# Optimization experiments

Hardware: AMD Instinct MI355X
Metric: run time of the kernel (lower is better)

## Reference

```python
import jax, jax.numpy as jnp
import numpy as np

N_NODES = 40000
N_EDGES = 640000
IN_DIM = 128
HID = 128
NCLS = 10
N_GRAPHS = 16
K = 2  # DGL TAGConv default number of hops


def setup_inputs() -> dict:
    key = jax.random.key(0)
    ks = jax.random.split(key, 8)
    h = jax.random.normal(ks[0], (N_NODES, IN_DIM), dtype=jnp.float32)
    src = jax.random.randint(ks[1], (N_EDGES,), 0, N_NODES, dtype=jnp.int64)
    dst = jax.random.randint(ks[2], (N_EDGES,), 0, N_NODES, dtype=jnp.int64)
    graph_ids = jnp.sort(jax.random.randint(ks[3], (N_NODES,), 0, N_GRAPHS, dtype=jnp.int64))
    # Xavier-ish scaled params
    W1 = jax.random.normal(ks[4], ((K + 1) * IN_DIM, HID), dtype=jnp.float32) / np.sqrt((K + 1) * IN_DIM)
    b1 = jnp.zeros((HID,), dtype=jnp.float32)
    W2 = jax.random.normal(ks[5], ((K + 1) * HID, HID), dtype=jnp.float32) / np.sqrt((K + 1) * HID)
    b2 = jnp.zeros((HID,), dtype=jnp.float32)
    Wc = jax.random.normal(ks[6], (HID, NCLS), dtype=jnp.float32) / np.sqrt(HID)
    bc = jnp.zeros((NCLS,), dtype=jnp.float32)
    return {"h": h, "src": src, "dst": dst, "graph_ids": graph_ids,
            "W1": W1, "b1": b1, "W2": W2, "b2": b2, "Wc": Wc, "bc": bc}


def _tagconv(x, src, dst, norm, W, b):
    feats = [x]
    for _ in range(K):
        msg = (x * norm)[src]                                   # [E, d] gather D^{-1/2} x at src
        x = norm * jax.ops.segment_sum(msg, dst, num_segments=norm.shape[0])  # scatter-sum to dst
        feats.append(x)
    return jax.nn.relu(jnp.concatenate(feats, axis=-1) @ W + b)


def reference(h, src, dst, graph_ids, W1, b1, W2, b2, Wc, bc):
    n = h.shape[0]
    deg = jax.ops.segment_sum(jnp.ones(src.shape[0], h.dtype), dst, num_segments=n)
    norm = jnp.maximum(deg, 1.0) ** -0.5  # D^{-1/2} with clamp(min=1), as in DGL
    norm = norm[:, None]
    x = _tagconv(h, src, dst, norm, W1, b1)
    x = _tagconv(x, src, dst, norm, W2, b2)
    pooled = jax.ops.segment_max(x, graph_ids, num_segments=N_GRAPHS)  # [G, HID] per-graph max pool
    return pooled @ Wc + bc  # [G, NCLS]
```

## Files before the change

### kernel.cpp

```cpp
#include <hip/hip_runtime.h>
#include <hip/hip_bf16.h>

#define NN 40000
#define NE 640000
#define HID 128
#define NCLS 10
#define NGRAPH 16

typedef __attribute__((ext_vector_type(8))) short bf16x8;
typedef __attribute__((ext_vector_type(4))) float f32x4;

__device__ inline float bf2f(unsigned short u) {
    unsigned int x = ((unsigned int)u) << 16;
    return __builtin_bit_cast(float, x);
}
__device__ inline unsigned short f2bf(float f) {
    __hip_bfloat16 h = __float2bfloat16(f);
    return __builtin_bit_cast(unsigned short, h);
}

__global__ void k_count_deg(const int* __restrict__ dst, int* __restrict__ deg, int n) {
    int e = blockIdx.x * blockDim.x + threadIdx.x;
    if (e < n) atomicAdd(&deg[__builtin_nontemporal_load(dst + e)], 1);
}

__global__ __launch_bounds__(1024) void k_scan1(const int* __restrict__ deg, int* __restrict__ row_start,
                                                int* __restrict__ partial, float* __restrict__ norm) {
    __shared__ int wsum[16];
    int tid = threadIdx.x, lane = tid & 63, wid = tid >> 6;
    int i = blockIdx.x * 1024 + tid;
    int v = (i < NN) ? deg[i] : 0;
    if (i < NN) norm[i] = rsqrtf(fmaxf((float)v, 1.0f));
    int sv = v;
    #pragma unroll
    for (int off = 1; off < 64; off <<= 1) {
        int t = __shfl_up(sv, off);
        if (lane >= off) sv += t;
    }
    if (lane == 63) wsum[wid] = sv;
    __syncthreads();
    if (wid == 0) {
        int ws = (lane < 16) ? wsum[lane] : 0;
        #pragma unroll
        for (int off = 1; off < 16; off <<= 1) {
            int t = __shfl_up(ws, off);
            if (lane >= off) ws += t;
        }
        if (lane < 16) wsum[lane] = ws;
    }
    __syncthreads();
    int excl = (wid > 0 ? wsum[wid - 1] : 0) + (sv - v);
    if (i < NN) row_start[i] = excl;
    if (tid == 0) partial[blockIdx.x] = wsum[15];
}

__global__ __launch_bounds__(1024) void k_scan3(int* __restrict__ row_start, const int* __restrict__ partial,
                                                int* __restrict__ cursor, int nb) {
    __shared__ int sh_carry, sh_all;
    int tid = threadIdx.x;
    if (tid < 64) {
        int v = (tid < nb) ? partial[tid] : 0;
        int lt = (tid < (int)blockIdx.x) ? v : 0;
        #pragma unroll
        for (int off = 32; off; off >>= 1) {
            lt += __shfl_down(lt, off);
            v  += __shfl_down(v, off);
        }
        if (tid == 0) { sh_carry = lt; sh_all = v; }
    }
    __syncthreads();
    int i = blockIdx.x * 1024 + tid;
    if (i < NN) {
        int val = row_start[i] + sh_carry;
        row_start[i] = val;
        cursor[i] = val;
    }
    if (blockIdx.x == 0 && tid == 0) row_start[NN] = sh_all;
}

__global__ void k_fill_csr(const int* __restrict__ src, const int* __restrict__ dst,
                           int* __restrict__ cursor, int* __restrict__ csr_src, int n) {
    int e = blockIdx.x * blockDim.x + threadIdx.x;
    if (e < n) {
        int d = __builtin_nontemporal_load(dst + e);
        int sv = __builtin_nontemporal_load(src + e);
        int pos = atomicAdd(&cursor[d], 1);
        csr_src[pos] = sv;
    }
}

__global__ void k_cvt_h(const float* __restrict__ h, unsigned short* __restrict__ hb) {
    int i = blockIdx.x * 256 + threadIdx.x;
    if (i < NN * HID / 4) {
        float4 v = reinterpret_cast<const float4*>(h)[i];
        ushort4 o;
        o.x = f2bf(v.x); o.y = f2bf(v.y); o.z = f2bf(v.z); o.w = f2bf(v.w);
        reinterpret_cast<ushort4*>(hb)[i] = o;
    }
}

__global__ void k_cvt_wt(const float* __restrict__ W1, const float* __restrict__ W2,
                         unsigned short* __restrict__ W1t, unsigned short* __restrict__ W2t) {
    int t = blockIdx.x * 256 + threadIdx.x;
    const float* W = blockIdx.y ? W2 : W1;
    unsigned short* Wt = blockIdx.y ? W2t : W1t;
    if (t < 384 * HID) {
        int c = t / 384, k = t % 384;
        Wt[t] = f2bf(W[(size_t)k * HID + c]);
    }
}

__global__ __launch_bounds__(256) void k_prop_bf(const unsigned short* __restrict__ x, const float* __restrict__ norm,
                                                 const int* __restrict__ row_start, const int* __restrict__ csr_src,
                                                 unsigned short* __restrict__ y) {
    int node = blockIdx.x * 4 + threadIdx.y;
    int lane = threadIdx.x;
    int h = lane >> 5;
    int sub = lane & 31;
    int colb = sub * 4;
    float a0 = 0.f, a1 = 0.f, a2 = 0.f, a3 = 0.f;
    int s = row_start[node], e = row_start[node + 1];
    int i = s + h;
    if (i + 6 < e) {
        int c0 = csr_src[i], c1 = csr_src[i + 2], c2 = csr_src[i + 4], c3 = csr_src[i + 6];
        int j = i + 8;
        while (true) {
            bool more = (j + 6 < e);
            int n0, n1, n2, n3;
            if (more) {
                n0 = csr_src[j]; n1 = csr_src[j + 2]; n2 = csr_src[j + 4]; n3 = csr_src[j + 6];
            }
            float s0 = norm[c0], s1 = norm[c1], s2 = norm[c2], s3 = norm[c3];
            ushort4 v0 = *reinterpret_cast<const ushort4*>(x + (size_t)c0 * HID + colb);
            ushort4 v1 = *reinterpret_cast<const ushort4*>(x + (size_t)c1 * HID + colb);
            ushort4 v2 = *reinterpret_cast<const ushort4*>(x + (size_t)c2 * HID + colb);
            ushort4 v3 = *reinterpret_cast<const ushort4*>(x + (size_t)c3 * HID + colb);
            a0 += s0 * bf2f(v0.x) + s1 * bf2f(v1.x) + s2 * bf2f(v2.x) + s3 * bf2f(v3.x);
            a1 += s0 * bf2f(v0.y) + s1 * bf2f(v1.y) + s2 * bf2f(v2.y) + s3 * bf2f(v3.y);
            a2 += s0 * bf2f(v0.z) + s1 * bf2f(v1.z) + s2 * bf2f(v2.z) + s3 * bf2f(v3.z);
            a3 += s0 * bf2f(v0.w) + s1 * bf2f(v1.w) + s2 * bf2f(v2.w) + s3 * bf2f(v3.w);
            i = j;
            if (!more) break;
            c0 = n0; c1 = n1; c2 = n2; c3 = n3;
            j += 8;
        }
    }
    for (; i < e; i += 2) {
        int sn = csr_src[i];
        float ns = norm[sn];
        ushort4 v = *reinterpret_cast<const ushort4*>(x + (size_t)sn * HID + colb);
        a0 += ns * bf2f(v.x); a1 += ns * bf2f(v.y); a2 += ns * bf2f(v.z); a3 += ns * bf2f(v.w);
    }
    a0 += __shfl_xor(a0, 32);
    a1 += __shfl_xor(a1, 32);
    a2 += __shfl_xor(a2, 32);
    a3 += __shfl_xor(a3, 32);
    if (h == 0) {
        float nd = norm[node];
        ushort4 o;
        o.x = f2bf(nd * a0); o.y = f2bf(nd * a1); o.z = f2bf(nd * a2); o.w = f2bf(nd * a3);
        *reinterpret_cast<ushort4*>(y + (size_t)node * HID + colb) = o;
    }
}

__global__ __launch_bounds__(128) void k_gemm_mfma(const unsigned short* __restrict__ x0,
                                                   const unsigned short* __restrict__ x1,
                                                   const unsigned short* __restrict__ x2,
                                                   const unsigned short* __restrict__ Wt,
                                                   const float* __restrict__ bias,
                                                   unsigned short* __restrict__ y) {
    int tid = threadIdx.x;
    int wave = tid >> 6;
    int lane = tid & 63;
    int r = lane & 15, kg = lane >> 4;
    int row0 = blockIdx.x * 32 + wave * 16;
    const unsigned short* xs[3] = { x0, x1, x2 };

    f32x4 acc[8];
    #pragma unroll
    for (int cf = 0; cf < 8; ++cf) acc[cf] = (f32x4){0.f, 0.f, 0.f, 0.f};

    #pragma unroll
    for (int kseg = 0; kseg < 3; ++kseg) {
        const unsigned short* __restrict__ xp = xs[kseg] + (size_t)(row0 + r) * HID;
        #pragma unroll
        for (int kb = 0; kb < 4; ++kb) {
            bf16x8 afrag = *reinterpret_cast<const bf16x8*>(xp + kb * 32 + kg * 8);
            #pragma unroll
            for (int cf = 0; cf < 8; ++cf) {
                bf16x8 bfrag = *reinterpret_cast<const bf16x8*>(
                    Wt + (size_t)(cf * 16 + r) * 384 + kseg * 128 + kb * 32 + kg * 8);
                acc[cf] = __builtin_amdgcn_mfma_f32_16x16x32_bf16(afrag, bfrag, acc[cf], 0, 0, 0);
            }
        }
    }
    int orow = row0 + (lane >> 4) * 4;
    int colr = lane & 15;
    #pragma unroll
    for (int cf = 0; cf < 8; ++cf) {
        int col = cf * 16 + colr;
        float bb = bias[col];
        #pragma unroll
        for (int v = 0; v < 4; ++v) {
            float val = fmaxf(acc[cf][v] + bb, 0.f);
            y[(size_t)(orow + v) * HID + col] = f2bf(val);
        }
    }
}

__global__ __launch_bounds__(128) void k_pool_bf(const unsigned short* __restrict__ Z, const int* __restrict__ gid,
                                                 float* __restrict__ pooled, int n) {
    const int CHUNK = 16;
    int d = threadIdx.x;
    int start = blockIdx.x * CHUNK;
    if (start >= n) return;
    int end = min(start + CHUNK, n);
    float m = 0.0f;
    int cg = gid[start];
    int i = start;
    for (; i + 2 <= end; i += 2) {
        int g0 = gid[i], g1 = gid[i + 1];
        float v0 = bf2f(Z[(size_t)i * HID + d]);
        float v1 = bf2f(Z[(size_t)(i + 1) * HID + d]);
        if (g0 != cg) {
            atomicMax((unsigned int*)&pooled[cg * HID + d], __float_as_uint(m));
            m = 0.0f; cg = g0;
        }
        m = fmaxf(m, v0);
        if (g1 != cg) {
            atomicMax((unsigned int*)&pooled[cg * HID + d], __float_as_uint(m));
            m = 0.0f; cg = g1;
        }
        m = fmaxf(m, v1);
    }
    for (; i < end; ++i) {
        int g = gid[i];
        if (g != cg) {
            atomicMax((unsigned int*)&pooled[cg * HID + d], __float_as_uint(m));
            m = 0.0f; cg = g;
        }
        m = fmaxf(m, bf2f(Z[(size_t)i * HID + d]));
    }
    atomicMax((unsigned int*)&pooled[cg * HID + d], __float_as_uint(m));
}

__global__ void k_head(const float* __restrict__ pooled, const float* __restrict__ Wc,
                       const float* __restrict__ bc, float* __restrict__ out) {
    int t = threadIdx.x;
    if (t < NGRAPH * NCLS) {
        int g = t / NCLS, c = t % NCLS;
        float acc = bc[c];
        for (int k = 0; k < HID; ++k) acc += pooled[g * HID + k] * Wc[k * NCLS + c];
        out[t] = acc;
    }
}

extern "C" void kernel_launch(void* const* d_in, const int* in_sizes, int n_in,
                              void* d_out, int out_size, void* d_ws, size_t ws_size,
                              hipStream_t stream) {
    const float* h   = (const float*)d_in[0];
    const int*   src = (const int*)d_in[1];
    const int*   dst = (const int*)d_in[2];
    const int*   gid = (const int*)d_in[3];
    const float* W1  = (const float*)d_in[4];
    const float* b1  = (const float*)d_in[5];
    const float* W2  = (const float*)d_in[6];
    const float* b2  = (const float*)d_in[7];
    const float* Wc  = (const float*)d_in[8];
    const float* bc  = (const float*)d_in[9];
    float* out = (float*)d_out;

    char* ws = (char*)d_ws;
    size_t off = 0;
    auto alloc = [&](size_t bytes) { void* p = ws + off; off = (off + bytes + 63) & ~(size_t)63; return p; };
    int*   deg       = (int*)alloc((size_t)NN * 4);
    int*   cursor    = (int*)alloc((size_t)NN * 4);
    int*   row_start = (int*)alloc((size_t)(NN + 1) * 4);
    int*   csr_src   = (int*)alloc((size_t)NE * 4);
    float* norm      = (float*)alloc((size_t)NN * 4);
    int*   partial   = (int*)alloc(64 * 4);
    float* pooled    = (float*)alloc((size_t)NGRAPH * HID * 4);
    unsigned short* W1t = (unsigned short*)alloc((size_t)384 * HID * 2);
    unsigned short* W2t = (unsigned short*)alloc((size_t)384 * HID * 2);
    const size_t FB = (size_t)NN * HID * 2;
    unsigned short* hb  = (unsigned short*)alloc(FB);
    unsigned short* Bb  = (unsigned short*)alloc(FB);
    unsigned short* Cb  = (unsigned short*)alloc(FB);
    unsigned short* Yb  = (unsigned short*)alloc(FB);
    unsigned short* Zb  = (unsigned short*)alloc(FB);

    hipMemsetAsync(deg, 0, (size_t)NN * 4, stream);
    hipMemsetAsync(pooled, 0, (size_t)NGRAPH * HID * 4, stream);

    const int EB = 256;
    const int SCAN_BLOCKS = (NN + 1023) / 1024;

    k_cvt_h<<<(NN * HID / 4 + 255) / 256, 256, 0, stream>>>(h, hb);
    dim3 wgrid((384 * HID + 255) / 256, 2);
    k_cvt_wt<<<wgrid, 256, 0, stream>>>(W1, W2, W1t, W2t);

    k_count_deg<<<(NE + EB - 1) / EB, EB, 0, stream>>>(dst, deg, NE);
    k_scan1<<<SCAN_BLOCKS, 1024, 0, stream>>>(deg, row_start, partial, norm);
    k_scan3<<<SCAN_BLOCKS, 1024, 0, stream>>>(row_start, partial, cursor, SCAN_BLOCKS);
    k_fill_csr<<<(NE + EB - 1) / EB, EB, 0, stream>>>(src, dst, cursor, csr_src, NE);

    dim3 pblk(64, 4);
    int pblocks = NN / 4;
    int gblocks = NN / 32;

    k_prop_bf<<<pblocks, pblk, 0, stream>>>(hb, norm, row_start, csr_src, Bb);
    k_prop_bf<<<pblocks, pblk, 0, stream>>>(Bb, norm, row_start, csr_src, Cb);
    k_gemm_mfma<<<gblocks, 128, 0, stream>>>(hb, Bb, Cb, W1t, b1, Yb);

    k_prop_bf<<<pblocks, pblk, 0, stream>>>(Yb, norm, row_start, csr_src, Bb);
    k_prop_bf<<<pblocks, pblk, 0, stream>>>(Bb, norm, row_start, csr_src, Cb);
    k_gemm_mfma<<<gblocks, 128, 0, stream>>>(Yb, Bb, Cb, W2t, b2, Zb);

    k_pool_bf<<<(NN + 15) / 16, 128, 0, stream>>>(Zb, gid, pooled, NN);
    k_head<<<1, 192, 0, stream>>>(pooled, Wc, bc, out);
}
```

Measured before the change: 279.5 us.

## Fuse max-pool into second GEMM epilogue and enlarge GEMM row tile

```diff
diff --git a/kernel.cpp b/kernel.cpp
--- a/kernel.cpp
+++ b/kernel.cpp
@@ -6,6 +6,8 @@
 #define HID 128
 #define NCLS 10
 #define NGRAPH 16
+#define GB 313
+#define NNP (GB * 128)
 
 typedef __attribute__((ext_vector_type(8))) short bf16x8;
 typedef __attribute__((ext_vector_type(4))) float f32x4;
@@ -163,85 +165,94 @@
     }
 }
 
-__global__ __launch_bounds__(128) void k_gemm_mfma(const unsigned short* __restrict__ x0,
+__global__ __launch_bounds__(256) void k_gemm_mfma(const unsigned short* __restrict__ x0,
                                                    const unsigned short* __restrict__ x1,
                                                    const unsigned short* __restrict__ x2,
                                                    const unsigned short* __restrict__ Wt,
                                                    const float* __restrict__ bias,
-                                                   unsigned short* __restrict__ y) {
+                                                   unsigned short* __restrict__ y,
+                                                   const int* __restrict__ gid,
+                                                   float* __restrict__ pooled) {
     int tid = threadIdx.x;
     int wave = tid >> 6;
     int lane = tid & 63;
     int r = lane & 15, kg = lane >> 4;
-    int row0 = blockIdx.x * 32 + wave * 16;
+    int row0 = blockIdx.x * 128 + wave * 32;
+    if (row0 >= NN) return;
     const unsigned short* xs[3] = { x0, x1, x2 };
 
-    f32x4 acc[8];
+    f32x4 acc[2][8];
     #pragma unroll
-    for (int cf = 0; cf < 8; ++cf) acc[cf] = (f32x4){0.f, 0.f, 0.f, 0.f};
+    for (int rf = 0; rf < 2; ++rf)
+        #pragma unroll
+        for (int cf = 0; cf < 8; ++cf) acc[rf][cf] = (f32x4){0.f, 0.f, 0.f, 0.f};
 
     #pragma unroll
     for (int kseg = 0; kseg < 3; ++kseg) {
-        const unsigned short* __restrict__ xp = xs[kseg] + (size_t)(row0 + r) * HID;
+        const unsigned short* __restrict__ xpA = xs[kseg] + (size_t)(row0 + r) * HID;
+        const unsigned short* __restrict__ xpB = xpA + 16 * HID;
         #pragma unroll
         for (int kb = 0; kb < 4; ++kb) {
-            bf16x8 afrag = *reinterpret_cast<const bf16x8*>(xp + kb * 32 + kg * 8);
+            bf16x8 a0 = *reinterpret_cast<const bf16x8*>(xpA + kb * 32 + kg * 8);
+            bf16x8 a1 = *reinterpret_cast<const bf16x8*>(xpB + kb * 32 + kg * 8);
             #pragma unroll
             for (int cf = 0; cf < 8; ++cf) {
-                bf16x8 bfrag = *reinterpret_cast<const bf16x8*>(
+                bf16x8 b = *reinterpret_cast<const bf16x8*>(
                     Wt + (size_t)(cf * 16 + r) * 384 + kseg * 128 + kb * 32 + kg * 8);
-                acc[cf] = __builtin_amdgcn_mfma_f32_16x16x32_bf16(afrag, bfrag, acc[cf], 0, 0, 0);
-            }
-        }
-    }
-    int orow = row0 + (lane >> 4) * 4;
+                acc[0][cf] = __builtin_amdgcn_mfma_f32_16x16x32_bf16(a0, b, acc[0][cf], 0, 0, 0);
+                acc[1][cf] = __builtin_amdgcn_mfma_f32_16x16x32_bf16(a1, b, acc[1][cf], 0, 0, 0);
+            }
+        }
+    }
     int colr = lane & 15;
+    int vb = (lane >> 4) * 4;
     #pragma unroll
-    for (int cf = 0; cf < 8; ++cf) {
-        int col = cf * 16 + colr;
-        float bb = bias[col];
-        #pragma unroll
-        for (int v = 0; v < 4; ++v) {
-            float val = fmaxf(acc[cf][v] + bb, 0.f);
-            y[(size_t)(orow + v) * HID + col] = f2bf(val);
-        }
-    }
-}
-
-__global__ __launch_bounds__(128) void k_pool_bf(const unsigned short* __restrict__ Z, const int* __restrict__ gid,
-                                                 float* __restrict__ pooled, int n) {
-    const int CHUNK = 16;
-    int d = threadIdx.x;
-    int start = blockIdx.x * CHUNK;
-    if (start >= n) return;
-    int end = min(start + CHUNK, n);
-    float m = 0.0f;
-    int cg = gid[start];
-    int i = start;
-    for (; i + 2 <= end; i += 2) {
-        int g0 = gid[i], g1 = gid[i + 1];
-        float v0 = bf2f(Z[(size_t)i * HID + d]);
-        float v1 = bf2f(Z[(size_t)(i + 1) * HID + d]);
-        if (g0 != cg) {
-            atomicMax((unsigned int*)&pooled[cg * HID + d], __float_as_uint(m));
-            m = 0.0f; cg = g0;
-        }
-        m = fmaxf(m, v0);
-        if (g1 != cg) {
-            atomicMax((unsigned int*)&pooled[cg * HID + d], __float_as_uint(m));
-            m = 0.0f; cg = g1;
-        }
-        m = fmaxf(m, v1);
-    }
-    for (; i < end; ++i) {
-        int g = gid[i];
-        if (g != cg) {
-            atomicMax((unsigned int*)&pooled[cg * HID + d], __float_as_uint(m));
-            m = 0.0f; cg = g;
-        }
-        m = fmaxf(m, bf2f(Z[(size_t)i * HID + d]));
-    }
-    atomicMax((unsigned int*)&pooled[cg * HID + d], __float_as_uint(m));
+    for (int rf = 0; rf < 2; ++rf) {
+        int orow = row0 + rf * 16 + vb;
+        if (y) {
+            #pragma unroll
+            for (int cf = 0; cf < 8; ++cf) {
+                int col = cf * 16 + colr;
+                float bb = bias[col];
+                #pragma unroll
+                for (int v = 0; v < 4; ++v) {
+                    int row = orow + v;
+                    if (row < NN) {
+                        float val = fmaxf(acc[rf][cf][v] + bb, 0.f);
+                        y[(size_t)row * HID + col] = f2bf(val);
+                    }
+                }
+            }
+        } else {
+            int gg[4];
+            #pragma unroll
+            for (int v = 0; v < 4; ++v) {
+                int row = orow + v;
+                gg[v] = (row < NN) ? gid[row] : -1;
+            }
+            #pragma unroll
+            for (int cf = 0; cf < 8; ++cf) {
+                int col = cf * 16 + colr;
+                float bb = bias[col];
+                float m = 0.f;
+                int cg = gg[0];
+                bool any = false;
+                #pragma unroll
+                for (int v = 0; v < 4; ++v) {
+                    if (gg[v] >= 0) {
+                        float val = fmaxf(acc[rf][cf][v] + bb, 0.f);
+                        if (gg[v] != cg) {
+                            if (any) atomicMax((unsigned int*)&pooled[cg * HID + col], __float_as_uint(m));
+                            m = 0.f; cg = gg[v];
+                        }
+                        m = fmaxf(m, val);
+                        any = true;
+                    }
+                }
+                if (any) atomicMax((unsigned int*)&pooled[cg * HID + col], __float_as_uint(m));
+            }
+        }
+    }
 }
 
 __global__ void k_head(const float* __restrict__ pooled, const float* __restrict__ Wc,
@@ -282,12 +293,11 @@
     float* pooled    = (float*)alloc((size_t)NGRAPH * HID * 4);
     unsigned short* W1t = (unsigned short*)alloc((size_t)384 * HID * 2);
     unsigned short* W2t = (unsigned short*)alloc((size_t)384 * HID * 2);
-    const size_t FB = (size_t)NN * HID * 2;
+    const size_t FB = (size_t)NNP * HID * 2;
     unsigned short* hb  = (unsigned short*)alloc(FB);
     unsigned short* Bb  = (unsigned short*)alloc(FB);
     unsigned short* Cb  = (unsigned short*)alloc(FB);
     unsigned short* Yb  = (unsigned short*)alloc(FB);
-    unsigned short* Zb  = (unsigned short*)alloc(FB);
 
     hipMemsetAsync(deg, 0, (size_t)NN * 4, stream);
     hipMemsetAsync(pooled, 0, (size_t)NGRAPH * HID * 4, stream);
@@ -306,16 +316,14 @@
 
     dim3 pblk(64, 4);
     int pblocks = NN / 4;
-    int gblocks = NN / 32;
 
     k_prop_bf<<<pblocks, pblk, 0, stream>>>(hb, norm, row_start, csr_src, Bb);
     k_prop_bf<<<pblocks, pblk, 0, stream>>>(Bb, norm, row_start, csr_src, Cb);
-    k_gemm_mfma<<<gblocks, 128, 0, stream>>>(hb, Bb, Cb, W1t, b1, Yb);
+    k_gemm_mfma<<<GB, 256, 0, stream>>>(hb, Bb, Cb, W1t, b1, Yb, nullptr, nullptr);
 
     k_prop_bf<<<pblocks, pblk, 0, stream>>>(Yb, norm, row_start, csr_src, Bb);
     k_prop_bf<<<pblocks, pblk, 0, stream>>>(Bb, norm, row_start, csr_src, Cb);
-    k_gemm_mfma<<<gblocks, 128, 0, stream>>>(Yb, Bb, Cb, W2t, b2, Zb);
-
-    k_pool_bf<<<(NN + 15) / 16, 128, 0, stream>>>(Zb, gid, pooled, NN);
+    k_gemm_mfma<<<GB, 256, 0, stream>>>(Yb, Bb, Cb, W2t, b2, nullptr, gid, pooled);
+
     k_head<<<1, 192, 0, stream>>>(pooled, Wc, bc, out);
 }
```

Measured after the change: 328.5 us. 1.18x slower.
